# Kernel tuning notes

Hardware: AMD Instinct MI355X
Metric: run time of the kernel (lower is better)

Reference implementation:

```python
import jax, jax.numpy as jnp
import numpy as np

# 26 neighbor taps of a 3x3x3 kernel in the exact order the torch module builds them:
# raster order over (z,y,x) in {0,1,2}^3, skipping the center (1,1,1).
OFFSETS = [(i, j, k) for i in range(3) for j in range(3) for k in range(3) if (i, j, k) != (1, 1, 1)]
DILATIONS = [1, 2]


def _affinity(x, d):
    # x: [B, K, D, H, W]; conv3d(kernel, dilation=d) on replicate-padded input is
    # exactly center-minus-shifted-neighbor with edge padding.
    B, K, D, H, W = x.shape
    xp = jnp.pad(x, ((0, 0), (0, 0), (d, d), (d, d), (d, d)), mode='edge')
    diffs = [x - xp[:, :, i * d:i * d + D, j * d:j * d + H * 0 + D if False else j * d + H, k * d:k * d + W]
             for (i, j, k) in OFFSETS]
    # fix slice bounds cleanly (depth D, height H, width W)
    diffs = [x - xp[:, :, i * d:i * d + D, j * d:j * d + H, k * d:k * d + W] for (i, j, k) in OFFSETS]
    return jnp.stack(diffs, axis=2)  # [B, K, 26, D, H, W]


def setup_inputs() -> dict:
    key = jax.random.key(0)
    x = jax.random.normal(key, (1, 2, 64, 128, 128), dtype=jnp.float32)
    return {"x": x}


def reference(x):
    # out: [B, K, 26*len(DILATIONS), D, H, W]
    affs = [_affinity(x, d) for d in DILATIONS]
    return jnp.concatenate(affs, axis=2)
```

## Files before the change

kernel.cpp:

```cpp
#include <hip/hip_runtime.h>


constexpr int Dz   = 64;
constexpr int Hy   = 128;
constexpr int Wx   = 128;
constexpr int HW   = Hy * Wx;
constexpr int DHW  = Dz * HW;
constexpr int TAPS = 52;

typedef float floatx4   __attribute__((ext_vector_type(4)));
typedef float floatx4_u __attribute__((ext_vector_type(4), aligned(4)));

__device__ __forceinline__ int iclamp(int v, int lo, int hi) {
    return v < lo ? lo : (v > hi ? hi : v);
}

__global__ __launch_bounds__(256)
void LocalAffinity_kernel(const float* __restrict__ in, float* __restrict__ out) {
    const int bid = blockIdx.x;
    const int q   = bid & 3;
    const int z   = (bid >> 2) & 63;
    const int b3  = bid >> 8;
    const int t   = b3 % TAPS;
    const int k   = b3 / TAPS;

    const int d   = (t < 26) ? 1 : 2;
    const int t26 = (t < 26) ? t : t - 26;
    const int ras = (t26 < 13) ? t26 : t26 + 1;
    const int di  = ras / 9 - 1;
    const int dj  = (ras % 9) / 3 - 1;
    const int dk  = (ras % 3) - 1;
    const int dkd = dk * d;
    const int dy  = dj * d;
    const int zc  = iclamp(z + di * d, 0, Dz - 1);

    const float* __restrict__ ctr = in + k * DHW + z  * HW;
    const float* __restrict__ src = in + k * DHW + zc * HW;

    const int tid = threadIdx.x;
    const int x4  = tid & 31;
    const int x0  = x4 << 2;
    const int yb  = (q << 5) | (tid >> 5);

    floatx4 c[4], s[4];
    #pragma unroll
    for (int p = 0; p < 4; ++p) {
        const int y = yb + (p << 3);
        c[p] = *(const floatx4*)(ctr + y * Wx + x0);
    }
    #pragma unroll
    for (int p = 0; p < 4; ++p) {
        const int y  = yb + (p << 3);
        const int yc = iclamp(y + dy, 0, Hy - 1);
        const float* row = src + yc * Wx;
        if (dkd == 0) {
            s[p] = *(const floatx4*)(row + x0);
        } else {
            const int xsa = iclamp(x0 + dkd, 0, Wx - 4);
            const floatx4 v = *(const floatx4_u*)(row + xsa);
            floatx4 sv = v;
            if (dkd < 0) {
                const bool e = (x4 == 0);
                if (dkd == -1) {
                    if (e) { sv.x = v.x; sv.y = v.x; sv.z = v.y; sv.w = v.z; }
                } else {
                    if (e) { sv.x = v.x; sv.y = v.x; sv.z = v.x; sv.w = v.y; }
                }
            } else {
                const bool e = (x4 == 31);
                if (dkd == 1) {
                    if (e) { sv.x = v.y; sv.y = v.z; sv.z = v.w; sv.w = v.w; }
                } else {
                    if (e) { sv.x = v.z; sv.y = v.w; sv.z = v.w; sv.w = v.w; }
                }
            }
            s[p] = sv;
        }
    }

    float* __restrict__ obase = out + (size_t)(k * TAPS + t) * (size_t)DHW
                                    + (size_t)z * HW;
    #pragma unroll
    for (int p = 0; p < 4; ++p) {
        const int y = yb + (p << 3);
        floatx4 r;
        r.x = c[p].x - s[p].x; r.y = c[p].y - s[p].y;
        r.z = c[p].z - s[p].z; r.w = c[p].w - s[p].w;
        __builtin_nontemporal_store(r, (floatx4*)(obase + y * Wx + x0));
    }
}

extern "C" void kernel_launch(void* const* d_in, const int* in_sizes, int n_in,
                              void* d_out, int out_size, void* d_ws, size_t ws_size,
                              hipStream_t stream) {
    const float* x = (const float*)d_in[0];
    float* out = (float*)d_out;
    LocalAffinity_kernel<<<2 * TAPS * Dz * 4, 256, 0, stream>>>(x, out);
}
```

Baseline: 422.3 us.

## Make kernel persistent with double-buffered register prefetch of next chunk

Replaces the one-chunk-per-block launch (26624 blocks) with 2048 persistent blocks that each process 13 chunks. While storing the current chunk, each block prefetches the next chunk's center and shifted loads into a second register buffer. The goal is to overlap load latency with the nontemporal stores and cut block launch overhead. In exchange it doubles register usage and may reduce occupancy. The edge-clamp fixup now happens at store time.

```diff
diff --git a/kernel.cpp b/kernel.cpp
--- a/kernel.cpp
+++ b/kernel.cpp
@@ -7,6 +7,8 @@
 constexpr int HW   = Hy * Wx;
 constexpr int DHW  = Dz * HW;
 constexpr int TAPS = 52;
+constexpr int NBLK  = 2048;
+constexpr int NITER = 13;
 
 typedef float floatx4   __attribute__((ext_vector_type(4)));
 typedef float floatx4_u __attribute__((ext_vector_type(4), aligned(4)));
@@ -15,15 +17,14 @@
     return v < lo ? lo : (v > hi ? hi : v);
 }
 
-__global__ __launch_bounds__(256)
-void LocalAffinity_kernel(const float* __restrict__ in, float* __restrict__ out) {
-    const int bid = blockIdx.x;
-    const int q   = bid & 3;
-    const int z   = (bid >> 2) & 63;
-    const int b3  = bid >> 8;
+__device__ __forceinline__ void load_chunk(const float* __restrict__ in,
+                                           int chunk, int tid,
+                                           floatx4* cc, floatx4* ss) {
+    const int q   = chunk & 3;
+    const int z   = (chunk >> 2) & 63;
+    const int b3  = chunk >> 8;
     const int t   = b3 % TAPS;
     const int k   = b3 / TAPS;
-
     const int d   = (t < 26) ? 1 : 2;
     const int t26 = (t < 26) ? t : t - 26;
     const int ras = (t26 < 13) ? t26 : t26 + 1;
@@ -34,59 +35,90 @@
     const int dy  = dj * d;
     const int zc  = iclamp(z + di * d, 0, Dz - 1);
 
-    const float* __restrict__ ctr = in + k * DHW + z  * HW;
-    const float* __restrict__ src = in + k * DHW + zc * HW;
+    const float* ctr = in + k * DHW + z  * HW;
+    const float* src = in + k * DHW + zc * HW;
+    const int x0 = (tid & 31) << 2;
+    const int yb = (q << 5) | (tid >> 5);
 
-    const int tid = threadIdx.x;
+    #pragma unroll
+    for (int p = 0; p < 4; ++p) {
+        const int y = yb + (p << 3);
+        cc[p] = *(const floatx4*)(ctr + y * Wx + x0);
+        const int yc = iclamp(y + dy, 0, Hy - 1);
+        const float* row = src + yc * Wx;
+        if (dkd == 0) {
+            ss[p] = *(const floatx4*)(row + x0);
+        } else {
+            const int xsa = iclamp(x0 + dkd, 0, Wx - 4);
+            ss[p] = *(const floatx4_u*)(row + xsa);
+        }
+    }
+}
+
+__device__ __forceinline__ void store_chunk(float* __restrict__ out,
+                                            int chunk, int tid,
+                                            const floatx4* cc, const floatx4* ss) {
+    const int q   = chunk & 3;
+    const int z   = (chunk >> 2) & 63;
+    const int b3  = chunk >> 8;
+    const int t   = b3 % TAPS;
+    const int k   = b3 / TAPS;
+    const int d   = (t < 26) ? 1 : 2;
+    const int t26 = (t < 26) ? t : t - 26;
+    const int ras = (t26 < 13) ? t26 : t26 + 1;
+    const int dk  = (ras % 3) - 1;
+    const int dkd = dk * d;
     const int x4  = tid & 31;
     const int x0  = x4 << 2;
     const int yb  = (q << 5) | (tid >> 5);
 
-    floatx4 c[4], s[4];
+    float* obase = out + (size_t)(k * TAPS + t) * (size_t)DHW + (size_t)z * HW;
+
     #pragma unroll
     for (int p = 0; p < 4; ++p) {
+        const floatx4 v = ss[p];
+        floatx4 sv = v;
+        if (dkd < 0) {
+            const bool e = (x4 == 0);
+            if (dkd == -1) {
+                if (e) { sv.x = v.x; sv.y = v.x; sv.z = v.y; sv.w = v.z; }
+            } else {
+                if (e) { sv.x = v.x; sv.y = v.x; sv.z = v.x; sv.w = v.y; }
+            }
+        } else if (dkd > 0) {
+            const bool e = (x4 == 31);
+            if (dkd == 1) {
+                if (e) { sv.x = v.y; sv.y = v.z; sv.z = v.w; sv.w = v.w; }
+            } else {
+                if (e) { sv.x = v.z; sv.y = v.w; sv.z = v.w; sv.w = v.w; }
+            }
+        }
+        const floatx4 c = cc[p];
+        floatx4 r;
+        r.x = c.x - sv.x; r.y = c.y - sv.y;
+        r.z = c.z - sv.z; r.w = c.w - sv.w;
         const int y = yb + (p << 3);
-        c[p] = *(const floatx4*)(ctr + y * Wx + x0);
+        __builtin_nontemporal_store(r, (floatx4*)(obase + y * Wx + x0));
     }
+}
+
+__global__ __launch_bounds__(256)
+void LocalAffinity_kernel(const float* __restrict__ in, float* __restrict__ out) {
+    const int bid = blockIdx.x;
+    const int tid = threadIdx.x;
+
+    floatx4 Ac[4], As[4], Bc[4], Bs[4];
+    load_chunk(in, bid, tid, Ac, As);
+
     #pragma unroll
-    for (int p = 0; p < 4; ++p) {
-        const int y  = yb + (p << 3);
-        const int yc = iclamp(y + dy, 0, Hy - 1);
-        const float* row = src + yc * Wx;
-        if (dkd == 0) {
-            s[p] = *(const floatx4*)(row + x0);
-        } else {
-            const int xsa = iclamp(x0 + dkd, 0, Wx - 4);
-            const floatx4 v = *(const floatx4_u*)(row + xsa);
-            floatx4 sv = v;
-            if (dkd < 0) {
-                const bool e = (x4 == 0);
-                if (dkd == -1) {
-                    if (e) { sv.x = v.x; sv.y = v.x; sv.z = v.y; sv.w = v.z; }
-                } else {
-                    if (e) { sv.x = v.x; sv.y = v.x; sv.z = v.x; sv.w = v.y; }
-                }
-            } else {
-                const bool e = (x4 == 31);
-                if (dkd == 1) {
-                    if (e) { sv.x = v.y; sv.y = v.z; sv.z = v.w; sv.w = v.w; }
-                } else {
-                    if (e) { sv.x = v.z; sv.y = v.w; sv.z = v.w; sv.w = v.w; }
-                }
-            }
-            s[p] = sv;
+    for (int it = 0; it < NITER; ++it) {
+        const int chunk = it * NBLK + bid;
+        if (it + 1 < NITER) {
+            if (it & 1) load_chunk(in, chunk + NBLK, tid, Ac, As);
+            else        load_chunk(in, chunk + NBLK, tid, Bc, Bs);
         }
-    }
-
-    float* __restrict__ obase = out + (size_t)(k * TAPS + t) * (size_t)DHW
-                                    + (size_t)z * HW;
-    #pragma unroll
-    for (int p = 0; p < 4; ++p) {
-        const int y = yb + (p << 3);
-        floatx4 r;
-        r.x = c[p].x - s[p].x; r.y = c[p].y - s[p].y;
-        r.z = c[p].z - s[p].z; r.w = c[p].w - s[p].w;
-        __builtin_nontemporal_store(r, (floatx4*)(obase + y * Wx + x0));
+        if (it & 1) store_chunk(out, chunk, tid, Bc, Bs);
+        else        store_chunk(out, chunk, tid, Ac, As);
     }
 }
 
@@ -95,5 +127,5 @@
                               hipStream_t stream) {
     const float* x = (const float*)d_in[0];
     float* out = (float*)d_out;
-    LocalAffinity_kernel<<<2 * TAPS * Dz * 4, 256, 0, stream>>>(x, out);
+    LocalAffinity_kernel<<<NBLK, 256, 0, stream>>>(x, out);
 }
```

Result: no change. 429.6 us (+1.7%).
